# Optimization experiments

Measured on AMD Instinct MI355X. Metric: run time of the kernel, lower is better.

The kernel has to match this reference:

```python
import jax, jax.numpy as jnp
import numpy as np

DIM = 768
HEADS = 12
HEAD_DIM = DIM // HEADS
HIDDEN = 4 * DIM
SCALE = HEAD_DIM ** -0.5
LN_EPS = 1e-5


def _fit_poly_gelu():
    # replicate PolyGELU.__init__: quadratic least-squares fit to exact GELU on [-3,3]
    x = np.linspace(-3.0, 3.0, 10000).astype(np.float32)
    y = np.asarray(jax.nn.gelu(jnp.asarray(x), approximate=False))
    X = np.stack([x ** 2, x, np.ones_like(x)], axis=1)
    c, *_ = np.linalg.lstsq(X, y, rcond=None)
    return c.astype(np.float32)  # [a, b, c]


def setup_inputs() -> dict:
    key = jax.random.key(0)
    ks = jax.random.split(key, 8)
    g = _fit_poly_gelu()
    w = lambda k, shp: (jax.random.normal(k, shp, dtype=jnp.float32) * 0.02)
    return {
        "x": jax.random.normal(ks[0], (4, 2048, DIM), dtype=jnp.float32),
        "ln1_g": jnp.ones((DIM,), jnp.float32),
        "ln1_b": jnp.zeros((DIM,), jnp.float32),
        "ln2_g": jnp.ones((DIM,), jnp.float32),
        "ln2_b": jnp.zeros((DIM,), jnp.float32),
        "qkv_w": w(ks[1], (DIM, 3 * DIM)),   # stored [in, out]
        "qkv_b": jnp.zeros((3 * DIM,), jnp.float32),
        "proj_w": w(ks[2], (DIM, DIM)),
        "proj_b": jnp.zeros((DIM,), jnp.float32),
        "fc1_w": w(ks[3], (DIM, HIDDEN)),
        "fc1_b": jnp.zeros((HIDDEN,), jnp.float32),
        "fc2_w": w(ks[4], (HIDDEN, DIM)),
        "fc2_b": jnp.zeros((DIM,), jnp.float32),
        "attn_a": jnp.float32(0.05),
        "attn_b": jnp.float32(0.5),
        "attn_c": jnp.float32(0.25),
        "gelu_a": jnp.float32(g[0]),
        "gelu_b": jnp.float32(g[1]),
        "gelu_c": jnp.float32(g[2]),
    }


def _layernorm(x, gamma, beta):
    mu = jnp.mean(x, axis=-1, keepdims=True)
    var = jnp.mean(jnp.square(x - mu), axis=-1, keepdims=True)
    return (x - mu) / jnp.sqrt(var + LN_EPS) * gamma + beta


def reference(x, ln1_g, ln1_b, ln2_g, ln2_b, qkv_w, qkv_b, proj_w, proj_b,
              fc1_w, fc1_b, fc2_w, fc2_b, attn_a, attn_b, attn_c,
              gelu_a, gelu_b, gelu_c):
    B, N, C = x.shape
    # --- attention branch ---
    h = _layernorm(x, ln1_g, ln1_b)
    qkv = (h @ qkv_w + qkv_b).reshape(B, N, 3, HEADS, HEAD_DIM)
    q, k, v = (qkv[:, :, i].transpose(0, 2, 1, 3) for i in range(3))  # [B,H,N,D]
    attn = jnp.einsum("bhnd,bhmd->bhnm", q, k) * SCALE
    # poly_normed: quadratic activation, clamp, row-normalize
    attn = attn_a * attn * attn + attn_b * attn + attn_c
    attn = jnp.maximum(attn, 1e-6)
    attn = attn / (jnp.sum(attn, axis=-1, keepdims=True) + 1e-8)
    out = jnp.einsum("bhnm,bhmd->bhnd", attn, v).transpose(0, 2, 1, 3).reshape(B, N, C)
    x = x + (out @ proj_w + proj_b)
    # --- MLP branch with PolyGELU ---
    h = _layernorm(x, ln2_g, ln2_b)
    u = h @ fc1_w + fc1_b
    u = gelu_a * u * u + gelu_b * u + gelu_c
    x = x + (u @ fc2_w + fc2_b)
    return x
```

## Files before the change

kernel.cpp:

```cpp
#include <hip/hip_runtime.h>

typedef __bf16 bf16x8 __attribute__((ext_vector_type(8)));
typedef __bf16 bf16x4 __attribute__((ext_vector_type(4)));
typedef float f32x4 __attribute__((ext_vector_type(4)));

#define LN_EPS 1e-5f

__device__ __forceinline__ void gl2lds16(const void* g, void* l) {
  __builtin_amdgcn_global_load_lds(
      (const __attribute__((address_space(1))) unsigned int*)g,
      (__attribute__((address_space(3))) unsigned int*)l, 16, 0, 0);
}

template <int KEEP>
__device__ __forceinline__ void pipe_barrier() {
  if constexpr (KEEP == 0)
    __asm__ __volatile__("s_waitcnt vmcnt(0) lgkmcnt(0)\n\ts_barrier" ::: "memory");
  else if constexpr (KEEP == 3)
    __asm__ __volatile__("s_waitcnt vmcnt(3) lgkmcnt(0)\n\ts_barrier" ::: "memory");
  else if constexpr (KEEP == 4)
    __asm__ __volatile__("s_waitcnt vmcnt(4) lgkmcnt(0)\n\ts_barrier" ::: "memory");
}

__global__ __launch_bounds__(256) void transpose_k(const float* __restrict__ in,
                                                   __bf16* __restrict__ out,
                                                   int R, int C) {
  __shared__ __bf16 t[32][33];
  int tx = threadIdx.x & 31, ty = threadIdx.x >> 5;
  int c = blockIdx.x * 32 + tx;
  for (int j = 0; j < 4; j++) {
    int r = blockIdx.y * 32 + ty + j * 8;
    t[ty + j * 8][tx] = (__bf16)in[(size_t)r * C + c];
  }
  __syncthreads();
  int r2 = blockIdx.y * 32 + tx;
  for (int j = 0; j < 4; j++) {
    int c2 = blockIdx.x * 32 + ty + j * 8;
    out[(size_t)c2 * R + r2] = t[tx][ty + j * 8];
  }
}

__global__ __launch_bounds__(256) void ln_kernel(const float* __restrict__ x,
                                                 const float* __restrict__ g,
                                                 const float* __restrict__ bta,
                                                 __bf16* __restrict__ out) {
  int row = blockIdx.x;
  size_t base = (size_t)row * 768;
  int t = threadIdx.x;
  float v[3];
  float s = 0.f, s2 = 0.f;
  for (int k = 0; k < 3; k++) {
    float f = x[base + t + k * 256];
    v[k] = f;
    s += f;
    s2 += f * f;
  }
  for (int m = 1; m < 64; m <<= 1) {
    s += __shfl_xor(s, m, 64);
    s2 += __shfl_xor(s2, m, 64);
  }
  __shared__ float sm[4][2];
  int wid = t >> 6, lane = t & 63;
  if (lane == 0) { sm[wid][0] = s; sm[wid][1] = s2; }
  __syncthreads();
  s = sm[0][0] + sm[1][0] + sm[2][0] + sm[3][0];
  s2 = sm[0][1] + sm[1][1] + sm[2][1] + sm[3][1];
  float mu = s * (1.f / 768.f);
  float var = s2 * (1.f / 768.f) - mu * mu;
  float rstd = rsqrtf(var + LN_EPS);
  for (int k = 0; k < 3; k++) {
    int c = t + k * 256;
    out[base + c] = (__bf16)((v[k] - mu) * rstd * g[c] + bta[c]);
  }
}

template <int MT, int NT, int EPI, bool SWAP, int WPB>
__global__ __launch_bounds__(256, WPB)
void gemm_pl(const __bf16* __restrict__ A, const __bf16* __restrict__ BT,
             const float* __restrict__ bias, const float* __restrict__ res,
             void* __restrict__ outv, __bf16* __restrict__ vtb,
             int M, int N, int K,
             const float* __restrict__ c0p, const float* __restrict__ c1p,
             const float* __restrict__ c2p) {
  __shared__ __bf16 As[3][MT][32];
  __shared__ __bf16 Bs[3][NT][32];
  constexpr int IW = MT / 32, JW = NT / 32;
  constexpr int S = MT / 64 + NT / 64;
  const int tid = threadIdx.x, lane = tid & 63, wid = tid >> 6;
  const int wr = wid >> 1, wc = wid & 1;
  const int mr = lane & 15, quad = lane >> 4;
  const int bx = SWAP ? blockIdx.y : blockIdx.x;
  const int by = SWAP ? blockIdx.x : blockIdx.y;
  const int m0 = by * MT, n0 = bx * NT;
  const int swzsrc = (((lane & 3) ^ ((lane >> 2) & 3)) * 8);
  const int srow = lane >> 2;
  const int ck = ((quad ^ (mr & 3)) * 8);

  f32x4 acc[IW][JW] = {};

  auto stage = [&](int k0, int buf) {
    for (int g = 0; g < MT / 64; g++) {
      int r0 = wid * (MT / 4) + g * 16 + srow;
      gl2lds16(&A[(size_t)(m0 + r0) * K + k0 + swzsrc], &As[buf][r0][(lane & 3) * 8]);
    }
    for (int g = 0; g < NT / 64; g++) {
      int r0 = wid * (NT / 4) + g * 16 + srow;
      gl2lds16(&BT[(size_t)(n0 + r0) * K + k0 + swzsrc], &Bs[buf][r0][(lane & 3) * 8]);
    }
  };

  const int T = K / 32;
  stage(0, 0);
  stage(32, 1);
  for (int it = 0; it < T; it++) {
    if (it < T - 1) pipe_barrier<S>(); else pipe_barrier<0>();
    if (it + 2 < T) stage((it + 2) * 32, (it + 2) % 3);
    const int pb = it % 3;
    bf16x8 af[IW], bfr[JW];
    for (int i = 0; i < IW; i++) af[i] = *(bf16x8*)&As[pb][wr * (MT / 2) + i * 16 + mr][ck];
    for (int j = 0; j < JW; j++) bfr[j] = *(bf16x8*)&Bs[pb][wc * (NT / 2) + j * 16 + mr][ck];
    for (int i = 0; i < IW; i++)
      for (int j = 0; j < JW; j++)
        acc[i][j] = __builtin_amdgcn_mfma_f32_16x16x32_bf16(af[i], bfr[j], acc[i][j], 0, 0, 0);
  }

  float ga = 0.f, gb = 0.f, gc = 0.f;
  if (EPI == 1) { ga = *c0p; gb = *c1p; gc = *c2p; }

  for (int i = 0; i < IW; i++) {
    for (int j = 0; j < JW; j++) {
      int col = n0 + wc * (NT / 2) + j * 16 + mr;
      float bv = bias[col];
      int row0 = m0 + wr * (MT / 2) + i * 16 + quad * 4;
      if (EPI == 3 && col >= 1536) {
        int hh = (col >> 6) - 24, dd = col & 63;
        bf16x4 pk;
        for (int r = 0; r < 4; r++) pk[r] = (__bf16)(acc[i][j][r] + bv);
        *(bf16x4*)&vtb[(((size_t)(row0 >> 11) * 12 + hh) * 64 + dd) * 2048 +
                       (row0 & 2047)] = pk;
      } else {
        for (int r = 0; r < 4; r++) {
          size_t idx = (size_t)(row0 + r) * N + col;
          float c = acc[i][j][r] + bv;
          if (EPI == 1) {
            float u = (ga * c + gb) * c + gc;
            ((__bf16*)outv)[idx] = (__bf16)u;
          } else if (EPI == 2) {
            ((float*)outv)[idx] = c + res[idx];
          } else {
            ((__bf16*)outv)[idx] = (__bf16)c;
          }
        }
      }
    }
  }
}

__global__ __launch_bounds__(256, 3) void attn_poly(const __bf16* __restrict__ qkv,
                                                    const __bf16* __restrict__ vt,
                                                    __bf16* __restrict__ outp,
                                                    const float* __restrict__ ap,
                                                    const float* __restrict__ bp,
                                                    const float* __restrict__ cp) {
  __shared__ __bf16 Ps[4][32][72];
  __shared__ __bf16 Kb[2][64][64];
  __shared__ __bf16 Vb[2][64][64];

  const int tid = threadIdx.x, lane = tid & 63, wid = tid >> 6;
  const int mr = lane & 15, quad = lane >> 4;
  const int q0 = blockIdx.x * 128;
  const int h = blockIdx.y, b = blockIdx.z;
  const int bh = b * 12 + h;
  const size_t baseQ = ((size_t)b * 2048) * 2304 + h * 64;

  const int swzsrc = (((lane & 7) ^ ((lane >> 3) & 7)) * 8);
  const int srow8 = lane >> 3;
  const int colS0 = ((quad ^ (mr & 7)) * 8);
  const int colS1 = (((4 + quad) ^ (mr & 7)) * 8);

  bf16x8 qf[2][2];
  for (int i = 0; i < 2; i++)
    for (int s = 0; s < 2; s++)
      qf[i][s] = *(const bf16x8*)&qkv[baseQ + (size_t)(q0 + wid * 32 + i * 16 + mr) * 2304 +
                                      s * 32 + quad * 8];

  const float a2 = (*ap) * 0.015625f, b2 = (*bp) * 0.125f, cc = *cp;
  f32x4 o_acc[2][4] = {};
  float l_acc[2] = {0.f, 0.f};

  auto stage = [&](int kt, int pb) {
    for (int g = 0; g < 2; g++) {
      int r0 = wid * 16 + g * 8 + srow8;
      gl2lds16(&qkv[baseQ + (size_t)(kt * 64 + r0) * 2304 + 768 + swzsrc],
               &Kb[pb][r0][(lane & 7) * 8]);
      gl2lds16(&vt[((size_t)bh * 64 + r0) * 2048 + kt * 64 + swzsrc],
               &Vb[pb][r0][(lane & 7) * 8]);
    }
  };

  stage(0, 0);
  int pb = 0;
  for (int kt = 0; kt < 32; kt++) {
    __syncthreads();
    if (kt < 31) stage(kt + 1, pb ^ 1);

    f32x4 sacc[2][4] = {};
    for (int j = 0; j < 4; j++) {
      for (int s = 0; s < 2; s++) {
        bf16x8 kf = *(bf16x8*)&Kb[pb][j * 16 + mr][s ? colS1 : colS0];
        for (int i = 0; i < 2; i++)
          sacc[i][j] = __builtin_amdgcn_mfma_f32_16x16x32_bf16(kf, qf[i][s], sacc[i][j], 0, 0, 0);
      }
    }
    for (int i = 0; i < 2; i++) {
      f32x4 racc = {0.f, 0.f, 0.f, 0.f};
      for (int j = 0; j < 4; j++) {
        f32x4 S = sacc[i][j];
        f32x4 p = (a2 * S + b2) * S + cc;
        p[0] = fmaxf(p[0], 1e-6f); p[1] = fmaxf(p[1], 1e-6f);
        p[2] = fmaxf(p[2], 1e-6f); p[3] = fmaxf(p[3], 1e-6f);
        racc += p;
        bf16x4 pk = {(__bf16)p[0], (__bf16)p[1], (__bf16)p[2], (__bf16)p[3]};
        *(bf16x4*)&Ps[wid][i * 16 + mr][j * 16 + quad * 4] = pk;
      }
      float rsum = racc[0] + racc[1] + racc[2] + racc[3];
      rsum += __shfl_xor(rsum, 16, 64);
      rsum += __shfl_xor(rsum, 32, 64);
      l_acc[i] += rsum;
    }

    __asm__ __volatile__("s_waitcnt lgkmcnt(0)" ::: "memory");

    for (int s = 0; s < 2; s++) {
      bf16x8 pf[2];
      for (int i = 0; i < 2; i++)
        pf[i] = *(bf16x8*)&Ps[wid][i * 16 + mr][s * 32 + quad * 8];
      for (int dt = 0; dt < 4; dt++) {
        bf16x8 vf = *(bf16x8*)&Vb[pb][dt * 16 + mr][s ? colS1 : colS0];
        for (int i = 0; i < 2; i++)
          o_acc[i][dt] = __builtin_amdgcn_mfma_f32_16x16x32_bf16(pf[i], vf, o_acc[i][dt], 0, 0, 0);
      }
    }
    __asm__ __volatile__("" ::: "memory");
    pb ^= 1;
  }

  size_t baseO = ((size_t)b * 2048) * 768 + h * 64;
  for (int i = 0; i < 2; i++) {
    float inv[4];
    for (int r = 0; r < 4; r++)
      inv[r] = 1.0f / (__shfl(l_acc[i], quad * 4 + r, 64) + 1e-8f);
    for (int dt = 0; dt < 4; dt++) {
      int q = q0 + wid * 32 + i * 16 + quad * 4;
      for (int r = 0; r < 4; r++)
        outp[baseO + (size_t)(q + r) * 768 + dt * 16 + mr] =
            (__bf16)(o_acc[i][dt][r] * inv[r]);
    }
  }
}

extern "C" void kernel_launch(void* const* d_in, const int* in_sizes, int n_in,
                              void* d_out, int out_size, void* d_ws, size_t ws_size,
                              hipStream_t stream) {
  const float* x     = (const float*)d_in[0];
  const float* ln1g  = (const float*)d_in[1];
  const float* ln1b  = (const float*)d_in[2];
  const float* ln2g  = (const float*)d_in[3];
  const float* ln2b  = (const float*)d_in[4];
  const float* qkvw  = (const float*)d_in[5];
  const float* qkvb  = (const float*)d_in[6];
  const float* projw = (const float*)d_in[7];
  const float* projb = (const float*)d_in[8];
  const float* fc1w  = (const float*)d_in[9];
  const float* fc1b  = (const float*)d_in[10];
  const float* fc2w  = (const float*)d_in[11];
  const float* fc2b  = (const float*)d_in[12];
  const float* attna = (const float*)d_in[13];
  const float* attnb = (const float*)d_in[14];
  const float* attnc = (const float*)d_in[15];
  const float* gelua = (const float*)d_in[16];
  const float* gelub = (const float*)d_in[17];
  const float* geluc = (const float*)d_in[18];

  char* ws = (char*)d_ws;
  __bf16* wT_qkv  = (__bf16*)(ws);
  __bf16* wT_proj = (__bf16*)(ws + 3538944);
  __bf16* wT_fc1  = (__bf16*)(ws + 4718592);
  __bf16* wT_fc2  = (__bf16*)(ws + 9437184);
  __bf16* h       = (__bf16*)(ws + 14155776);
  float*  x1      = (float*)(ws + 26738688);
  __bf16* qkvbuf  = (__bf16*)(ws + 51904512);
  __bf16* u       = (__bf16*)(ws + 51904512);
  __bf16* vtbuf   = (__bf16*)(ws + 89653248);
  float*  outp    = (float*)d_out;

  transpose_k<<<dim3(2304 / 32, 768 / 32), 256, 0, stream>>>(qkvw, wT_qkv, 768, 2304);
  transpose_k<<<dim3(768 / 32, 768 / 32), 256, 0, stream>>>(projw, wT_proj, 768, 768);
  transpose_k<<<dim3(3072 / 32, 768 / 32), 256, 0, stream>>>(fc1w, wT_fc1, 768, 3072);
  transpose_k<<<dim3(768 / 32, 3072 / 32), 256, 0, stream>>>(fc2w, wT_fc2, 3072, 768);

  ln_kernel<<<8192, 256, 0, stream>>>(x, ln1g, ln1b, h);
  gemm_pl<128, 128, 3, false, 3><<<dim3(18, 64), 256, 0, stream>>>(
      h, wT_qkv, qkvb, nullptr, qkvbuf, vtbuf, 8192, 2304, 768, nullptr, nullptr, nullptr);
  attn_poly<<<dim3(16, 12, 4), 256, 0, stream>>>(qkvbuf, vtbuf, h, attna, attnb, attnc);
  gemm_pl<64, 128, 2, true, 4><<<dim3(128, 6), 256, 0, stream>>>(
      h, wT_proj, projb, x, x1, nullptr, 8192, 768, 768, nullptr, nullptr, nullptr);
  ln_kernel<<<8192, 256, 0, stream>>>(x1, ln2g, ln2b, h);
  gemm_pl<128, 128, 1, false, 3><<<dim3(24, 64), 256, 0, stream>>>(
      h, wT_fc1, fc1b, nullptr, u, nullptr, 8192, 3072, 768, gelua, gelub, geluc);
  gemm_pl<64, 128, 2, true, 4><<<dim3(128, 6), 256, 0, stream>>>(
      u, wT_fc2, fc2b, x1, outp, nullptr, 8192, 768, 3072, nullptr, nullptr, nullptr);
}
```

Measured before the change: 410.4 us.

## Keep attention probabilities in registers via permlane swaps instead of LDS round-trip

The attention kernel no longer writes the poly-normalized probability tile to shared memory and reads it back as the MFMA A operand. Instead it packs pairs to bf16 with v_cvt_pk_bf16_f32 and reshuffles lanes with v_permlane32/16_swap so the S accumulator layout becomes the PV operand layout directly. This removes the per-tile LDS store, wait and load, and cuts shared memory use, which may allow higher occupancy. The grid is also reordered so batch-head is the fast dimension, which changes how blocks are scheduled and how K/V tiles are reused in cache. Correctness depends on the lane permutation matching the operand layout exactly.

Measured after the change: 399.0 us. 2.8% less time.

```diff
diff --git a/kernel.cpp b/kernel.cpp
--- a/kernel.cpp
+++ b/kernel.cpp
@@ -3,6 +3,7 @@
 typedef __bf16 bf16x8 __attribute__((ext_vector_type(8)));
 typedef __bf16 bf16x4 __attribute__((ext_vector_type(4)));
 typedef float f32x4 __attribute__((ext_vector_type(4)));
+typedef unsigned int u32x4v __attribute__((ext_vector_type(4)));
 
 #define LN_EPS 1e-5f
 
@@ -20,6 +21,18 @@
     __asm__ __volatile__("s_waitcnt vmcnt(3) lgkmcnt(0)\n\ts_barrier" ::: "memory");
   else if constexpr (KEEP == 4)
     __asm__ __volatile__("s_waitcnt vmcnt(4) lgkmcnt(0)\n\ts_barrier" ::: "memory");
+}
+
+__device__ __forceinline__ unsigned cvt_pk_bf16(float lo, float hi) {
+  unsigned r;
+  asm("v_cvt_pk_bf16_f32 %0, %1, %2" : "=v"(r) : "v"(lo), "v"(hi));
+  return r;
+}
+__device__ __forceinline__ void plane32_swap(unsigned& a, unsigned& b) {
+  asm("v_permlane32_swap_b32 %0, %1" : "+v"(a), "+v"(b));
+}
+__device__ __forceinline__ void plane16_swap(unsigned& a, unsigned& b) {
+  asm("v_permlane16_swap_b32 %0, %1" : "+v"(a), "+v"(b));
 }
 
 __global__ __launch_bounds__(256) void transpose_k(const float* __restrict__ in,
@@ -162,15 +175,14 @@
                                                     const float* __restrict__ ap,
                                                     const float* __restrict__ bp,
                                                     const float* __restrict__ cp) {
-  __shared__ __bf16 Ps[4][32][72];
   __shared__ __bf16 Kb[2][64][64];
   __shared__ __bf16 Vb[2][64][64];
 
   const int tid = threadIdx.x, lane = tid & 63, wid = tid >> 6;
   const int mr = lane & 15, quad = lane >> 4;
-  const int q0 = blockIdx.x * 128;
-  const int h = blockIdx.y, b = blockIdx.z;
-  const int bh = b * 12 + h;
+  const int bh = blockIdx.x;
+  const int h = bh % 12, b = bh / 12;
+  const int q0 = blockIdx.y * 128;
   const size_t baseQ = ((size_t)b * 2048) * 2304 + h * 64;
 
   const int swzsrc = (((lane & 7) ^ ((lane >> 3) & 7)) * 8);
@@ -212,7 +224,10 @@
           sacc[i][j] = __builtin_amdgcn_mfma_f32_16x16x32_bf16(kf, qf[i][s], sacc[i][j], 0, 0, 0);
       }
     }
+
+    bf16x8 pf[2][2];
     for (int i = 0; i < 2; i++) {
+      unsigned w0[4], w1[4];
       f32x4 racc = {0.f, 0.f, 0.f, 0.f};
       for (int j = 0; j < 4; j++) {
         f32x4 S = sacc[i][j];
@@ -220,28 +235,30 @@
         p[0] = fmaxf(p[0], 1e-6f); p[1] = fmaxf(p[1], 1e-6f);
         p[2] = fmaxf(p[2], 1e-6f); p[3] = fmaxf(p[3], 1e-6f);
         racc += p;
-        bf16x4 pk = {(__bf16)p[0], (__bf16)p[1], (__bf16)p[2], (__bf16)p[3]};
-        *(bf16x4*)&Ps[wid][i * 16 + mr][j * 16 + quad * 4] = pk;
+        w0[j] = cvt_pk_bf16(p[0], p[1]);
+        w1[j] = cvt_pk_bf16(p[2], p[3]);
       }
       float rsum = racc[0] + racc[1] + racc[2] + racc[3];
       rsum += __shfl_xor(rsum, 16, 64);
       rsum += __shfl_xor(rsum, 32, 64);
       l_acc[i] += rsum;
-    }
-
-    __asm__ __volatile__("s_waitcnt lgkmcnt(0)" ::: "memory");
+      for (int s = 0; s < 2; s++) {
+        unsigned a0 = w0[2 * s], b0 = w0[2 * s + 1];
+        unsigned a1 = w1[2 * s], b1 = w1[2 * s + 1];
+        plane32_swap(a0, b0); plane16_swap(a0, b0);
+        plane32_swap(a1, b1); plane16_swap(a1, b1);
+        u32x4v t = {a0, a1, b0, b1};
+        pf[i][s] = __builtin_bit_cast(bf16x8, t);
+      }
+    }
 
     for (int s = 0; s < 2; s++) {
-      bf16x8 pf[2];
-      for (int i = 0; i < 2; i++)
-        pf[i] = *(bf16x8*)&Ps[wid][i * 16 + mr][s * 32 + quad * 8];
       for (int dt = 0; dt < 4; dt++) {
         bf16x8 vf = *(bf16x8*)&Vb[pb][dt * 16 + mr][s ? colS1 : colS0];
         for (int i = 0; i < 2; i++)
-          o_acc[i][dt] = __builtin_amdgcn_mfma_f32_16x16x32_bf16(pf[i], vf, o_acc[i][dt], 0, 0, 0);
-      }
-    }
-    __asm__ __volatile__("" ::: "memory");
+          o_acc[i][dt] = __builtin_amdgcn_mfma_f32_16x16x32_bf16(pf[i][s], vf, o_acc[i][dt], 0, 0, 0);
+      }
+    }
     pb ^= 1;
   }
 
@@ -302,7 +319,7 @@
   ln_kernel<<<8192, 256, 0, stream>>>(x, ln1g, ln1b, h);
   gemm_pl<128, 128, 3, false, 3><<<dim3(18, 64), 256, 0, stream>>>(
       h, wT_qkv, qkvb, nullptr, qkvbuf, vtbuf, 8192, 2304, 768, nullptr, nullptr, nullptr);
-  attn_poly<<<dim3(16, 12, 4), 256, 0, stream>>>(qkvbuf, vtbuf, h, attna, attnb, attnc);
+  attn_poly<<<dim3(48, 16), 256, 0, stream>>>(qkvbuf, vtbuf, h, attna, attnb, attnc);
   gemm_pl<64, 128, 2, true, 4><<<dim3(128, 6), 256, 0, stream>>>(
       h, wT_proj, projb, x, x1, nullptr, 8192, 768, 768, nullptr, nullptr, nullptr);
   ln_kernel<<<8192, 256, 0, stream>>>(x1, ln2g, ln2b, h);
```
